# Kernel tuning notes

Measured on AMD Instinct MI355X. Metric: run time of the kernel, lower is better.

## Reference

```python
import jax, jax.numpy as jnp
import numpy as np

N_NODES = 50000


def _sage_conv(x, src, dst, w_l, b_l, w_r):
    """PyG SAGEConv with mean aggregation: lin_l(mean_j x_j) + lin_r(x_i)."""
    msg = x[src]  # [E, d] gather from source nodes
    agg = jax.ops.segment_sum(msg, dst, num_segments=N_NODES)  # [N, d]
    deg = jax.ops.segment_sum(jnp.ones(dst.shape, dtype=x.dtype), dst, num_segments=N_NODES)
    agg = agg / jnp.maximum(deg, 1.0)[:, None]  # mean, zero-degree safe
    return agg @ w_l + b_l + x @ w_r


def setup_inputs() -> dict:
    key = jax.random.key(0)
    ks = jax.random.split(key, 6)
    in_dim, hid, out = 128, 512, 40
    x = jax.random.normal(ks[0], (N_NODES, in_dim), dtype=jnp.float32)
    edge_index = jax.random.randint(ks[1], (2, 800000), 0, N_NODES, dtype=jnp.int64)
    s1 = 1.0 / np.sqrt(in_dim)
    s2 = 1.0 / np.sqrt(hid)
    return {
        "x": x,
        "edge_index": edge_index,
        "w1_l": jax.random.normal(ks[2], (in_dim, hid), dtype=jnp.float32) * s1,
        "b1": jnp.zeros((hid,), dtype=jnp.float32),
        "w1_r": jax.random.normal(ks[3], (in_dim, hid), dtype=jnp.float32) * s1,
        "w2_l": jax.random.normal(ks[4], (hid, out), dtype=jnp.float32) * s2,
        "b2": jnp.zeros((out,), dtype=jnp.float32),
        "w2_r": jax.random.normal(ks[5], (hid, out), dtype=jnp.float32) * s2,
    }


def reference(x, edge_index, w1_l, b1, w1_r, w2_l, b2, w2_r):
    src, dst = edge_index[0], edge_index[1]
    h = _sage_conv(x, src, dst, w1_l, b1, w1_r)
    h = jax.nn.relu(h)  # dropout is identity at inference
    h = _sage_conv(h, src, dst, w2_l, b2, w2_r)
    return jax.nn.log_softmax(h, axis=1)
```

## Files before the change

kernel.cpp:

```cpp
#include <hip/hip_runtime.h>
#include <math.h>

#define N_NODES 50000
#define N_EDGES 800000
#define IN_DIM 128
#define HID 512
#define OUT_DIM 40
#define NRANGE 8
#define RANGE_SZ ((N_NODES + NRANGE - 1) / NRANGE)
#define NCHUNK 250
#define PER_CHUNK 3200
#define CAP 64

#define FILL_BLKS (NRANGE * NCHUNK)
#define CVTX_BLKS 6250
#define CVTW_BLKS 672
#define FUSED_BLKS (FILL_BLKS + CVTX_BLKS + CVTW_BLKS)

typedef __attribute__((ext_vector_type(8))) short bf16x8;
typedef __attribute__((ext_vector_type(4))) float f32x4;
typedef __attribute__((ext_vector_type(4))) int i32x4;

__device__ __forceinline__ ushort f2bf(float f) {
    unsigned u = __float_as_uint(f);
    u += 0x7fff + ((u >> 16) & 1);
    return (ushort)(u >> 16);
}

__device__ __forceinline__ float bf2f(ushort u) {
    return __uint_as_float(((unsigned)u) << 16);
}

__device__ __forceinline__ void gload_lds16(const ushort* g, ushort* l) {
    __builtin_amdgcn_global_load_lds(
        (__attribute__((address_space(1))) void*)g,
        (__attribute__((address_space(3))) void*)l, 16, 0, 0);
}

__global__ void fill_and_prep(
    const int* __restrict__ src, const int* __restrict__ dst,
    int* __restrict__ cursor, ushort* __restrict__ csr,
    const float* __restrict__ x, ushort* __restrict__ abuf,
    const float* __restrict__ w1l, const float* __restrict__ w1r,
    const float* __restrict__ w2l, const float* __restrict__ w2r,
    ushort* __restrict__ wt, ushort* __restrict__ wt2) {
    int b = blockIdx.x, t = threadIdx.x;
    if (b < FILL_BLKS) {
        int range = b & (NRANGE - 1);
        int chunk = b >> 3;
        int lo = range * RANGE_SZ;
        int hi = lo + RANGE_SZ; if (hi > N_NODES) hi = N_NODES;
        int beg = chunk * PER_CHUNK;
        for (int e = beg + t * 4; e < beg + PER_CHUNK; e += 1024) {
            i32x4 d4 = *(const i32x4*)(dst + e);
            i32x4 s4 = *(const i32x4*)(src + e);
            if (d4.x >= lo && d4.x < hi) {
                int pos = atomicAdd(&cursor[d4.x], 1);
                if (pos < CAP) csr[d4.x * CAP + pos] = (ushort)s4.x;
            }
            if (d4.y >= lo && d4.y < hi) {
                int pos = atomicAdd(&cursor[d4.y], 1);
                if (pos < CAP) csr[d4.y * CAP + pos] = (ushort)s4.y;
            }
            if (d4.z >= lo && d4.z < hi) {
                int pos = atomicAdd(&cursor[d4.z], 1);
                if (pos < CAP) csr[d4.z * CAP + pos] = (ushort)s4.z;
            }
            if (d4.w >= lo && d4.w < hi) {
                int pos = atomicAdd(&cursor[d4.w], 1);
                if (pos < CAP) csr[d4.w * CAP + pos] = (ushort)s4.w;
            }
        }
    } else if (b < FILL_BLKS + CVTX_BLKS) {
        int i = (b - FILL_BLKS) * 256 + t;
        int n = i >> 5, q = i & 31;
        float4 v = *(const float4*)(x + (size_t)n * 128 + q * 4);
        ushort4 o;
        o.x = f2bf(v.x); o.y = f2bf(v.y); o.z = f2bf(v.z); o.w = f2bf(v.w);
        *(ushort4*)(abuf + (size_t)n * 256 + 128 + q * 4) = o;
    } else {
        int i = (b - FILL_BLKS - CVTX_BLKS) * 256 + t;
        if (i < 512 * 256) {
            int k = i >> 9, c = i & 511;
            float v = (k < 128) ? w1l[(size_t)k * 512 + c] : w1r[(size_t)(k - 128) * 512 + c];
            wt[(size_t)c * 256 + k] = f2bf(v);
        } else {
            int j = i - 512 * 256;
            int c = j >> 9, k = j & 511;
            float v = (c < 40) ? w2l[(size_t)k * 40 + c] : w2r[(size_t)k * 40 + (c - 40)];
            wt2[(size_t)c * 512 + k] = f2bf(v);
        }
    }
}

__global__ void agg_x(const int* __restrict__ cursor,
                      const ushort* __restrict__ csr, ushort* __restrict__ abuf) {
    int wid = threadIdx.x >> 6;
    int lane = threadIdx.x & 63;
    int n = blockIdx.x * 4 + wid;
    if (n >= N_NODES) return;
    int d = cursor[n]; if (d > CAP) d = CAP;
    int beg = n * CAP, end = beg + d;
    int half = lane >> 5, l32 = lane & 31;
    const ushort* xb = abuf + 128;
    float a0 = 0, a1 = 0, a2 = 0, a3 = 0;
    float b0 = 0, b1 = 0, b2_ = 0, b3 = 0;
    int e = beg + half;
    for (; e + 2 < end; e += 4) {
        int s0 = csr[e], s1 = csr[e + 2];
        ushort4 v0 = *(const ushort4*)(xb + (size_t)s0 * 256 + l32 * 4);
        ushort4 v1 = *(const ushort4*)(xb + (size_t)s1 * 256 + l32 * 4);
        a0 += bf2f(v0.x); a1 += bf2f(v0.y); a2 += bf2f(v0.z); a3 += bf2f(v0.w);
        b0 += bf2f(v1.x); b1 += bf2f(v1.y); b2_ += bf2f(v1.z); b3 += bf2f(v1.w);
    }
    if (e < end) {
        int s = csr[e];
        ushort4 v = *(const ushort4*)(xb + (size_t)s * 256 + l32 * 4);
        a0 += bf2f(v.x); a1 += bf2f(v.y); a2 += bf2f(v.z); a3 += bf2f(v.w);
    }
    a0 += b0; a1 += b1; a2 += b2_; a3 += b3;
    a0 += __shfl_xor(a0, 32);
    a1 += __shfl_xor(a1, 32);
    a2 += __shfl_xor(a2, 32);
    a3 += __shfl_xor(a3, 32);
    if (d < 1) d = 1;
    float inv = 1.0f / (float)d;
    if (half == 0) {
        ushort4 o;
        o.x = f2bf(a0 * inv); o.y = f2bf(a1 * inv);
        o.z = f2bf(a2 * inv); o.w = f2bf(a3 * inv);
        *(ushort4*)(abuf + (size_t)n * 256 + l32 * 4) = o;
    }
}

#define EPI_LD 136
__global__ __launch_bounds__(256) void gemm1_mfma(
    const ushort* __restrict__ A, const ushort* __restrict__ BT,
    const float* __restrict__ bias, ushort* __restrict__ h) {
    __shared__ ushort pool[128 * EPI_LD];
    ushort* As = pool;
    ushort* Bs = pool + 8192;
    int tid = threadIdx.x;
    int wave = tid >> 6, lane = tid & 63;
    int wm = wave >> 1, wn = wave & 1;
    int nwg = gridDim.x;
    int q = nwg >> 3, r = nwg & 7;
    int xcd = blockIdx.x & 7, pos = blockIdx.x >> 3;
    int base = (xcd < r) ? xcd * (q + 1) : r * (q + 1) + (xcd - r) * q;
    int id = base + pos;
    int row0 = (id >> 2) * 128;
    int col0 = (id & 3) * 128;

    f32x4 acc[4][4] = {};
    for (int kk = 0; kk < 256; kk += 64) {
        #pragma unroll
        for (int c = 0; c < 4; ++c) {
            int ch = wave + c * 4;
            int o = ch * 1024 + lane * 16;
            int row = o >> 7;
            int s = (o >> 4) & 7;
            int ssrc = s ^ (row & 7);
            int gr = row0 + row; if (gr > N_NODES - 1) gr = N_NODES - 1;
            gload_lds16(A + (size_t)gr * 256 + kk + (ssrc << 3), As + ch * 512);
            int gc = col0 + row;
            gload_lds16(BT + (size_t)gc * 256 + kk + (ssrc << 3), Bs + ch * 512);
        }
        __syncthreads();
        #pragma unroll
        for (int kc = 0; kc < 2; ++kc) {
            int sbase = kc * 4 + (lane >> 4);
            bf16x8 af[4], bfr[4];
            #pragma unroll
            for (int m = 0; m < 4; ++m) {
                int row = wm * 64 + m * 16 + (lane & 15);
                af[m] = *(const bf16x8*)(As + row * 64 + ((sbase ^ (row & 7)) << 3));
            }
            #pragma unroll
            for (int n = 0; n < 4; ++n) {
                int row = wn * 64 + n * 16 + (lane & 15);
                bfr[n] = *(const bf16x8*)(Bs + row * 64 + ((sbase ^ (row & 7)) << 3));
            }
            #pragma unroll
            for (int m = 0; m < 4; ++m)
                #pragma unroll
                for (int n = 0; n < 4; ++n)
                    acc[m][n] = __builtin_amdgcn_mfma_f32_16x16x32_bf16(af[m], bfr[n], acc[m][n], 0, 0, 0);
        }
        __syncthreads();
    }

    #pragma unroll
    for (int n = 0; n < 4; ++n) {
        int col_l = wn * 64 + n * 16 + (lane & 15);
        float b = bias[col0 + col_l];
        #pragma unroll
        for (int m = 0; m < 4; ++m) {
            #pragma unroll
            for (int j = 0; j < 4; ++j) {
                int row_l = wm * 64 + m * 16 + (lane >> 4) * 4 + j;
                pool[row_l * EPI_LD + col_l] = f2bf(fmaxf(acc[m][n][j] + b, 0.f));
            }
        }
    }
    __syncthreads();
    #pragma unroll
    for (int it = 0; it < 8; ++it) {
        int idx = tid + it * 256;
        int row = idx >> 4, ch = idx & 15;
        int grow = row0 + row;
        if (grow < N_NODES) {
            int4 v = *(const int4*)(pool + row * EPI_LD + ch * 8);
            *(int4*)(h + (size_t)grow * 512 + col0 + ch * 8) = v;
        }
    }
}

__global__ __launch_bounds__(256) void gemm2_mfma(
    const ushort* __restrict__ hbf, const ushort* __restrict__ wt2,
    ushort* __restrict__ p, float* __restrict__ r) {
    __shared__ ushort As[2][128 * 64];
    __shared__ ushort Bs[2][80 * 64];
    int tid = threadIdx.x;
    int wave = tid >> 6, lane = tid & 63;
    int row0 = blockIdx.x * 128;
    f32x4 acc[2][5] = {};

    auto stage = [&](int buf, int kk) {
        #pragma unroll
        for (int c = 0; c < 4; ++c) {
            int ch = wave + c * 4;
            int o = ch * 1024 + lane * 16;
            int row = o >> 7;
            int s = (o >> 4) & 7;
            int ssrc = s ^ (row & 7);
            int gr = row0 + row; if (gr > N_NODES - 1) gr = N_NODES - 1;
            gload_lds16(hbf + (size_t)gr * 512 + kk + (ssrc << 3), As[buf] + ch * 512);
        }
        for (int ch = wave; ch < 10; ch += 4) {
            int o = ch * 1024 + lane * 16;
            int row = o >> 7;
            int s = (o >> 4) & 7;
            int ssrc = s ^ (row & 7);
            gload_lds16(wt2 + (size_t)row * 512 + kk + (ssrc << 3), Bs[buf] + ch * 512);
        }
    };

    stage(0, 0);
    __syncthreads();
    #pragma unroll
    for (int t = 0; t < 8; ++t) {
        int cur = t & 1;
        if (t < 7) stage(cur ^ 1, (t + 1) * 64);
        #pragma unroll
        for (int kc = 0; kc < 2; ++kc) {
            int sbase = kc * 4 + (lane >> 4);
            bf16x8 af[2], bfr[5];
            #pragma unroll
            for (int m = 0; m < 2; ++m) {
                int row = wave * 32 + m * 16 + (lane & 15);
                af[m] = *(const bf16x8*)(As[cur] + row * 64 + ((sbase ^ (row & 7)) << 3));
            }
            #pragma unroll
            for (int n = 0; n < 5; ++n) {
                int row = n * 16 + (lane & 15);
                bfr[n] = *(const bf16x8*)(Bs[cur] + row * 64 + ((sbase ^ (row & 7)) << 3));
            }
            #pragma unroll
            for (int m = 0; m < 2; ++m)
                #pragma unroll
                for (int n = 0; n < 5; ++n)
                    acc[m][n] = __builtin_amdgcn_mfma_f32_16x16x32_bf16(af[m], bfr[n], acc[m][n], 0, 0, 0);
        }
        __syncthreads();
    }
    #pragma unroll
    for (int m = 0; m < 2; ++m) {
        #pragma unroll
        for (int j = 0; j < 4; ++j) {
            int grow = row0 + wave * 32 + m * 16 + (lane >> 4) * 4 + j;
            if (grow >= N_NODES) continue;
            #pragma unroll
            for (int n = 0; n < 5; ++n) {
                int col = n * 16 + (lane & 15);
                float v = acc[m][n][j];
                if (col < 40) p[(size_t)grow * 40 + col] = f2bf(v);
                else          r[(size_t)grow * 40 + (col - 40)] = v;
            }
        }
    }
}

__global__ void final_kernel(const ushort* __restrict__ p, const float* __restrict__ rr,
                             const float* __restrict__ b2,
                             const int* __restrict__ cursor, const ushort* __restrict__ csr,
                             float* __restrict__ out) {
    int wid = threadIdx.x >> 6;
    int lane = threadIdx.x & 63;
    int n = blockIdx.x * 4 + wid;
    if (n >= N_NODES) return;
    int d = cursor[n]; if (d > CAP) d = CAP;
    int beg = n * CAP, end = beg + d;
    float acc0 = 0.f, acc1 = 0.f, acc2 = 0.f, acc3 = 0.f;
    int e = beg;
    if (lane < OUT_DIM) {
        for (; e + 3 < end; e += 4) {
            int s0 = csr[e], s1 = csr[e + 1];
            int s2 = csr[e + 2], s3 = csr[e + 3];
            acc0 += bf2f(p[(size_t)s0 * OUT_DIM + lane]);
            acc1 += bf2f(p[(size_t)s1 * OUT_DIM + lane]);
            acc2 += bf2f(p[(size_t)s2 * OUT_DIM + lane]);
            acc3 += bf2f(p[(size_t)s3 * OUT_DIM + lane]);
        }
        for (; e < end; ++e)
            acc0 += bf2f(p[(size_t)csr[e] * OUT_DIM + lane]);
    }
    if (d < 1) d = 1;
    float inv = 1.0f / (float)d;
    float v = (lane < OUT_DIM)
                  ? ((acc0 + acc1 + acc2 + acc3) * inv + b2[lane] + rr[(size_t)n * OUT_DIM + lane])
                  : -INFINITY;
    float m = v;
    #pragma unroll
    for (int off = 32; off; off >>= 1) m = fmaxf(m, __shfl_xor(m, off));
    float ex = (lane < OUT_DIM) ? expf(v - m) : 0.f;
    float ssum = ex;
    #pragma unroll
    for (int off = 32; off; off >>= 1) ssum += __shfl_xor(ssum, off);
    if (lane < OUT_DIM) out[(size_t)n * OUT_DIM + lane] = (v - m) - logf(ssum);
}

extern "C" void kernel_launch(void* const* d_in, const int* in_sizes, int n_in,
                              void* d_out, int out_size, void* d_ws, size_t ws_size,
                              hipStream_t stream) {
    const float* x    = (const float*)d_in[0];
    const int*   edge = (const int*)d_in[1];
    const int*   srce = edge;
    const int*   dste = edge + N_EDGES;
    const float* w1l  = (const float*)d_in[2];
    const float* b1   = (const float*)d_in[3];
    const float* w1r  = (const float*)d_in[4];
    const float* w2l  = (const float*)d_in[5];
    const float* b2   = (const float*)d_in[6];
    const float* w2r  = (const float*)d_in[7];
    float* out = (float*)d_out;

    char* ws = (char*)d_ws;
    size_t off = 0;
    auto alloc = [&](size_t bytes) -> void* {
        void* ptr = ws + off;
        off = (off + bytes + 255) & ~(size_t)255;
        return ptr;
    };
    int* cursor  = (int*)alloc((size_t)N_NODES * 4);
    ushort* csr  = (ushort*)alloc((size_t)N_NODES * CAP * 2);
    ushort* abuf = (ushort*)alloc((size_t)N_NODES * 256 * 2);
    ushort* wt   = (ushort*)alloc((size_t)512 * 256 * 2);
    ushort* wt2  = (ushort*)alloc((size_t)80 * 512 * 2);
    ushort* h    = (ushort*)alloc((size_t)N_NODES * HID * 2);
    ushort* p    = (ushort*)alloc((size_t)N_NODES * OUT_DIM * 2);
    float* rbuf  = (float*)alloc((size_t)N_NODES * OUT_DIM * 4);

    hipMemsetAsync(cursor, 0, (size_t)N_NODES * 4, stream);
    fill_and_prep<<<FUSED_BLKS, 256, 0, stream>>>(srce, dste, cursor, csr,
                                                  x, abuf, w1l, w1r, w2l, w2r, wt, wt2);
    agg_x<<<(N_NODES + 3) / 4, 256, 0, stream>>>(cursor, csr, abuf);
    gemm1_mfma<<<4 * ((N_NODES + 127) / 128), 256, 0, stream>>>(abuf, wt, b1, h);
    gemm2_mfma<<<(N_NODES + 127) / 128, 256, 0, stream>>>(h, wt2, p, rbuf);
    final_kernel<<<(N_NODES + 3) / 4, 256, 0, stream>>>(p, rbuf, b2, cursor, csr, out);
}
```

Baseline: 161.3 us.

## Fuse layer-1 and layer-2 GEMMs, keeping hidden tile in LDS

```diff
diff --git a/kernel.cpp b/kernel.cpp
--- a/kernel.cpp
+++ b/kernel.cpp
@@ -73,11 +73,11 @@
         }
     } else if (b < FILL_BLKS + CVTX_BLKS) {
         int i = (b - FILL_BLKS) * 256 + t;
-        int n = i >> 5, q = i & 31;
-        float4 v = *(const float4*)(x + (size_t)n * 128 + q * 4);
+        int n = i >> 5, qq = i & 31;
+        float4 v = *(const float4*)(x + (size_t)n * 128 + qq * 4);
         ushort4 o;
         o.x = f2bf(v.x); o.y = f2bf(v.y); o.z = f2bf(v.z); o.w = f2bf(v.w);
-        *(ushort4*)(abuf + (size_t)n * 256 + 128 + q * 4) = o;
+        *(ushort4*)(abuf + (size_t)n * 256 + 128 + qq * 4) = o;
     } else {
         int i = (b - FILL_BLKS - CVTX_BLKS) * 256 + t;
         if (i < 512 * 256) {
@@ -134,155 +134,106 @@
 }
 
 #define EPI_LD 136
-__global__ __launch_bounds__(256) void gemm1_mfma(
-    const ushort* __restrict__ A, const ushort* __restrict__ BT,
-    const float* __restrict__ bias, ushort* __restrict__ h) {
-    __shared__ ushort pool[128 * EPI_LD];
-    ushort* As = pool;
-    ushort* Bs = pool + 8192;
+__global__ __launch_bounds__(256) void gemm_fused(
+    const ushort* __restrict__ A, const ushort* __restrict__ WT,
+    const ushort* __restrict__ WT2, const float* __restrict__ bias,
+    ushort* __restrict__ p, float* __restrict__ r) {
+    __shared__ ushort As[128 * 64];
+    __shared__ ushort Bs[128 * 64];
+    __shared__ ushort hbuf[128 * EPI_LD];
     int tid = threadIdx.x;
     int wave = tid >> 6, lane = tid & 63;
     int wm = wave >> 1, wn = wave & 1;
-    int nwg = gridDim.x;
-    int q = nwg >> 3, r = nwg & 7;
-    int xcd = blockIdx.x & 7, pos = blockIdx.x >> 3;
-    int base = (xcd < r) ? xcd * (q + 1) : r * (q + 1) + (xcd - r) * q;
-    int id = base + pos;
-    int row0 = (id >> 2) * 128;
-    int col0 = (id & 3) * 128;
-
-    f32x4 acc[4][4] = {};
-    for (int kk = 0; kk < 256; kk += 64) {
+    int r16 = lane & 15, q = lane >> 4;
+    int row0 = blockIdx.x * 128;
+
+    f32x4 acc2[2][5] = {};
+
+    for (int cc = 0; cc < 4; ++cc) {
+        f32x4 acc1[4][4] = {};
+        for (int kk = 0; kk < 256; kk += 64) {
+            #pragma unroll
+            for (int c = 0; c < 4; ++c) {
+                int ch = wave + c * 4;
+                int o = ch * 1024 + lane * 16;
+                int row = o >> 7;
+                int s = (o >> 4) & 7;
+                int ssrc = s ^ (row & 7);
+                int gr = row0 + row; if (gr > N_NODES - 1) gr = N_NODES - 1;
+                gload_lds16(A + (size_t)gr * 256 + kk + (ssrc << 3), As + ch * 512);
+                int gc = cc * 128 + row;
+                gload_lds16(WT + (size_t)gc * 256 + kk + (ssrc << 3), Bs + ch * 512);
+            }
+            __syncthreads();
+            #pragma unroll
+            for (int kc = 0; kc < 2; ++kc) {
+                int sbase = kc * 4 + q;
+                bf16x8 af[4], bfr[4];
+                #pragma unroll
+                for (int m = 0; m < 4; ++m) {
+                    int row = wm * 64 + m * 16 + r16;
+                    af[m] = *(const bf16x8*)(As + row * 64 + ((sbase ^ (row & 7)) << 3));
+                }
+                #pragma unroll
+                for (int n = 0; n < 4; ++n) {
+                    int row = wn * 64 + n * 16 + r16;
+                    bfr[n] = *(const bf16x8*)(Bs + row * 64 + ((sbase ^ (row & 7)) << 3));
+                }
+                #pragma unroll
+                for (int m = 0; m < 4; ++m)
+                    #pragma unroll
+                    for (int n = 0; n < 4; ++n)
+                        acc1[m][n] = __builtin_amdgcn_mfma_f32_16x16x32_bf16(af[m], bfr[n], acc1[m][n], 0, 0, 0);
+            }
+            __syncthreads();
+        }
+
         #pragma unroll
-        for (int c = 0; c < 4; ++c) {
-            int ch = wave + c * 4;
-            int o = ch * 1024 + lane * 16;
-            int row = o >> 7;
-            int s = (o >> 4) & 7;
-            int ssrc = s ^ (row & 7);
-            int gr = row0 + row; if (gr > N_NODES - 1) gr = N_NODES - 1;
-            gload_lds16(A + (size_t)gr * 256 + kk + (ssrc << 3), As + ch * 512);
-            int gc = col0 + row;
-            gload_lds16(BT + (size_t)gc * 256 + kk + (ssrc << 3), Bs + ch * 512);
+        for (int n = 0; n < 4; ++n) {
+            int col_l = wn * 64 + n * 16 + r16;
+            float b = bias[cc * 128 + col_l];
+            #pragma unroll
+            for (int m = 0; m < 4; ++m) {
+                #pragma unroll
+                for (int j = 0; j < 4; ++j) {
+                    int row_l = wm * 64 + m * 16 + q * 4 + j;
+                    hbuf[row_l * EPI_LD + col_l] = f2bf(fmaxf(acc1[m][n][j] + b, 0.f));
+                }
+            }
         }
         __syncthreads();
+
         #pragma unroll
-        for (int kc = 0; kc < 2; ++kc) {
-            int sbase = kc * 4 + (lane >> 4);
-            bf16x8 af[4], bfr[4];
-            #pragma unroll
-            for (int m = 0; m < 4; ++m) {
-                int row = wm * 64 + m * 16 + (lane & 15);
-                af[m] = *(const bf16x8*)(As + row * 64 + ((sbase ^ (row & 7)) << 3));
-            }
-            #pragma unroll
-            for (int n = 0; n < 4; ++n) {
-                int row = wn * 64 + n * 16 + (lane & 15);
-                bfr[n] = *(const bf16x8*)(Bs + row * 64 + ((sbase ^ (row & 7)) << 3));
-            }
-            #pragma unroll
-            for (int m = 0; m < 4; ++m)
-                #pragma unroll
-                for (int n = 0; n < 4; ++n)
-                    acc[m][n] = __builtin_amdgcn_mfma_f32_16x16x32_bf16(af[m], bfr[n], acc[m][n], 0, 0, 0);
+        for (int kw = 0; kw < 4; ++kw) {
+            bf16x8 af2[2], bf2v[5];
+            #pragma unroll
+            for (int m = 0; m < 2; ++m) {
+                int row = wave * 32 + m * 16 + r16;
+                af2[m] = *(const bf16x8*)(hbuf + row * EPI_LD + kw * 32 + q * 8);
+            }
+            #pragma unroll
+            for (int n = 0; n < 5; ++n)
+                bf2v[n] = *(const bf16x8*)(WT2 + (size_t)(n * 16 + r16) * 512
+                                           + cc * 128 + kw * 32 + q * 8);
+            #pragma unroll
+            for (int m = 0; m < 2; ++m)
+                #pragma unroll
+                for (int n = 0; n < 5; ++n)
+                    acc2[m][n] = __builtin_amdgcn_mfma_f32_16x16x32_bf16(af2[m], bf2v[n], acc2[m][n], 0, 0, 0);
         }
         __syncthreads();
     }
 
-    #pragma unroll
-    for (int n = 0; n < 4; ++n) {
-        int col_l = wn * 64 + n * 16 + (lane & 15);
-        float b = bias[col0 + col_l];
-        #pragma unroll
-        for (int m = 0; m < 4; ++m) {
-            #pragma unroll
-            for (int j = 0; j < 4; ++j) {
-                int row_l = wm * 64 + m * 16 + (lane >> 4) * 4 + j;
-                pool[row_l * EPI_LD + col_l] = f2bf(fmaxf(acc[m][n][j] + b, 0.f));
-            }
-        }
-    }
-    __syncthreads();
-    #pragma unroll
-    for (int it = 0; it < 8; ++it) {
-        int idx = tid + it * 256;
-        int row = idx >> 4, ch = idx & 15;
-        int grow = row0 + row;
-        if (grow < N_NODES) {
-            int4 v = *(const int4*)(pool + row * EPI_LD + ch * 8);
-            *(int4*)(h + (size_t)grow * 512 + col0 + ch * 8) = v;
-        }
-    }
-}
-
-__global__ __launch_bounds__(256) void gemm2_mfma(
-    const ushort* __restrict__ hbf, const ushort* __restrict__ wt2,
-    ushort* __restrict__ p, float* __restrict__ r) {
-    __shared__ ushort As[2][128 * 64];
-    __shared__ ushort Bs[2][80 * 64];
-    int tid = threadIdx.x;
-    int wave = tid >> 6, lane = tid & 63;
-    int row0 = blockIdx.x * 128;
-    f32x4 acc[2][5] = {};
-
-    auto stage = [&](int buf, int kk) {
-        #pragma unroll
-        for (int c = 0; c < 4; ++c) {
-            int ch = wave + c * 4;
-            int o = ch * 1024 + lane * 16;
-            int row = o >> 7;
-            int s = (o >> 4) & 7;
-            int ssrc = s ^ (row & 7);
-            int gr = row0 + row; if (gr > N_NODES - 1) gr = N_NODES - 1;
-            gload_lds16(hbf + (size_t)gr * 512 + kk + (ssrc << 3), As[buf] + ch * 512);
-        }
-        for (int ch = wave; ch < 10; ch += 4) {
-            int o = ch * 1024 + lane * 16;
-            int row = o >> 7;
-            int s = (o >> 4) & 7;
-            int ssrc = s ^ (row & 7);
-            gload_lds16(wt2 + (size_t)row * 512 + kk + (ssrc << 3), Bs[buf] + ch * 512);
-        }
-    };
-
-    stage(0, 0);
-    __syncthreads();
-    #pragma unroll
-    for (int t = 0; t < 8; ++t) {
-        int cur = t & 1;
-        if (t < 7) stage(cur ^ 1, (t + 1) * 64);
-        #pragma unroll
-        for (int kc = 0; kc < 2; ++kc) {
-            int sbase = kc * 4 + (lane >> 4);
-            bf16x8 af[2], bfr[5];
-            #pragma unroll
-            for (int m = 0; m < 2; ++m) {
-                int row = wave * 32 + m * 16 + (lane & 15);
-                af[m] = *(const bf16x8*)(As[cur] + row * 64 + ((sbase ^ (row & 7)) << 3));
-            }
-            #pragma unroll
-            for (int n = 0; n < 5; ++n) {
-                int row = n * 16 + (lane & 15);
-                bfr[n] = *(const bf16x8*)(Bs[cur] + row * 64 + ((sbase ^ (row & 7)) << 3));
-            }
-            #pragma unroll
-            for (int m = 0; m < 2; ++m)
-                #pragma unroll
-                for (int n = 0; n < 5; ++n)
-                    acc[m][n] = __builtin_amdgcn_mfma_f32_16x16x32_bf16(af[m], bfr[n], acc[m][n], 0, 0, 0);
-        }
-        __syncthreads();
-    }
     #pragma unroll
     for (int m = 0; m < 2; ++m) {
         #pragma unroll
         for (int j = 0; j < 4; ++j) {
-            int grow = row0 + wave * 32 + m * 16 + (lane >> 4) * 4 + j;
+            int grow = row0 + wave * 32 + m * 16 + q * 4 + j;
             if (grow >= N_NODES) continue;
             #pragma unroll
             for (int n = 0; n < 5; ++n) {
-                int col = n * 16 + (lane & 15);
-                float v = acc[m][n][j];
+                int col = n * 16 + r16;
+                float v = acc2[m][n][j];
                 if (col < 40) p[(size_t)grow * 40 + col] = f2bf(v);
                 else          r[(size_t)grow * 40 + (col - 40)] = v;
             }
@@ -356,7 +307,6 @@
     ushort* abuf = (ushort*)alloc((size_t)N_NODES * 256 * 2);
     ushort* wt   = (ushort*)alloc((size_t)512 * 256 * 2);
     ushort* wt2  = (ushort*)alloc((size_t)80 * 512 * 2);
-    ushort* h    = (ushort*)alloc((size_t)N_NODES * HID * 2);
     ushort* p    = (ushort*)alloc((size_t)N_NODES * OUT_DIM * 2);
     float* rbuf  = (float*)alloc((size_t)N_NODES * OUT_DIM * 4);
 
@@ -364,7 +314,6 @@
     fill_and_prep<<<FUSED_BLKS, 256, 0, stream>>>(srce, dste, cursor, csr,
                                                   x, abuf, w1l, w1r, w2l, w2r, wt, wt2);
     agg_x<<<(N_NODES + 3) / 4, 256, 0, stream>>>(cursor, csr, abuf);
-    gemm1_mfma<<<4 * ((N_NODES + 127) / 128), 256, 0, stream>>>(abuf, wt, b1, h);
-    gemm2_mfma<<<(N_NODES + 127) / 128, 256, 0, stream>>>(h, wt2, p, rbuf);
+    gemm_fused<<<(N_NODES + 127) / 128, 256, 0, stream>>>(abuf, wt, wt2, b1, p, rbuf);
     final_kernel<<<(N_NODES + 3) / 4, 256, 0, stream>>>(p, rbuf, b2, cursor, csr, out);
 }
```

Result: slower. 165.6 us (+2.7%).
